# Kernel optimization log

Hardware: AMD Instinct MI355X
Metric: run time of the kernel (lower is better)

The kernel has to match this reference:

```python
import jax, jax.numpy as jnp
import numpy as np


def _resize_hw(x, h, w):
    # PyTorch F.interpolate(mode='bilinear', align_corners=False) == half-pixel
    # bilinear without antialiasing.
    return jax.image.resize(x, x.shape[:-2] + (h, w), method='bilinear', antialias=False)


def _make_char_mask(attn, fore_mask, alpha):
    # attn: [b,26,w_attn] float; fore_mask: [b,1,H,W] int32
    W = fore_mask.shape[-1]
    attn_i = _resize_hw(attn[:, None], 26, W)[:, 0]          # [b,26,W]
    attn_b = (attn_i > alpha).astype(jnp.int32)              # threshold
    single = attn_b[:, :, None, :] * fore_mask               # [b,26,H,W]
    return jnp.concatenate([1 - fore_mask, single], axis=1)  # [b,27,H,W]


def _loss(char_feature, mask, length):
    # char_feature: [b,27,H,W] logits; mask: [b,27,H,W] int; length: [b]
    c = char_feature.shape[1]
    target = jnp.argmax(mask, axis=1)                         # [b,H,W] (first-max, same as torch)
    logp = jax.nn.log_softmax(char_feature, axis=1)
    ce = -jnp.mean(jnp.take_along_axis(logp, target[:, None], axis=1))
    prob = jnp.exp(logp)
    m = mask.astype(prob.dtype)
    smooth = 1.0
    inter = jnp.sum(prob * m, axis=(2, 3))                    # [b,27]
    s1 = jnp.sum(prob, axis=(2, 3))
    s2 = jnp.sum(m, axis=(2, 3))
    score = (2.0 * inter + smooth) / (s1 + s2 + smooth)       # [b,27]
    lens = length - 1                                          # chars per sample
    ch = jnp.arange(c)
    valid = (ch[None, :] >= 1) & (ch[None, :] <= lens[:, None])  # channels 1..len
    per_sample = jnp.sum((1.0 - score) * valid, axis=1) / lens.astype(prob.dtype)
    dice = jnp.mean(per_sample)
    return ce + dice


def setup_inputs() -> dict:
    key = jax.random.key(0)
    k1, k2, k3, k4, k5 = jax.random.split(key, 5)
    b = 512
    return {
        'char_feature_mid': jax.random.normal(k1, (b, 27, 32, 128), dtype=jnp.float32),
        'char_feature_low': jax.random.normal(k2, (b, 27, 16, 64), dtype=jnp.float32),
        'seq1_attention_map': jax.random.uniform(k3, (b, 26, 32), dtype=jnp.float32),
        'fore_mask': jax.random.uniform(k4, (b, 1, 32, 128), dtype=jnp.float32),
        'length': jax.random.randint(k5, (b,), 2, 27),
        'alpha': jnp.float32(0.3),
    }


def reference(char_feature_mid, char_feature_low, seq1_attention_map, fore_mask, length, alpha):
    h_mid, w_mid = char_feature_mid.shape[-2:]
    h_low, w_low = char_feature_low.shape[-2:]
    # clear_noise: zero attention rows at index >= length-1
    keep = jnp.arange(seq1_attention_map.shape[1])[None, :] < (length - 1)[:, None]
    attn = seq1_attention_map * keep[..., None].astype(seq1_attention_map.dtype)
    # low-resolution branch
    fm_low = (_resize_hw(fore_mask, h_low, w_low) >= 0.4).astype(jnp.int32)
    mask_low = _make_char_mask(attn, fm_low, alpha)
    loss_low = _loss(char_feature_low, mask_low, length)
    # middle-resolution branch
    fm_mid = (_resize_hw(fore_mask, h_mid, w_mid) >= 0.4).astype(jnp.int32)
    mask_mid = _make_char_mask(attn, fm_mid, alpha)
    loss_middle = _loss(char_feature_mid, mask_mid, length)
    return ((loss_low, loss_middle), mask_low)
```

## Files before the change

### kernel.cpp

```cpp
#include <hip/hip_runtime.h>
#include <stdint.h>


static __device__ __forceinline__ float wave_reduce_add(float v) {
  v += __shfl_xor(v, 1, 64);
  v += __shfl_xor(v, 2, 64);
  v += __shfl_xor(v, 4, 64);
  v += __shfl_xor(v, 8, 64);
  v += __shfl_xor(v, 16, 64);
  v += __shfl_xor(v, 32, 64);
  return v;
}

static __device__ __forceinline__ uint32_t attn_bits(const float* sattn, float src,
                                                     int lens, float alpha) {
  const int k0 = (int)floorf(src);
  uint32_t bits = 0u;
  if (k0 < 0 || k0 >= 31) {
    const int kk = (k0 < 0) ? 0 : 31;
    for (int c = 0; c < 26; ++c) {
      float v = (c < lens) ? sattn[c * 32 + kk] : 0.0f;
      if (v > alpha) bits |= (1u << c);
    }
  } else {
    const float frac = src - (float)k0;
    const float w1 = frac, w0 = 1.0f - frac;
    for (int c = 0; c < 26; ++c) {
      float v = __fadd_rn(__fmul_rn(w0, sattn[c * 32 + k0]),
                          __fmul_rn(w1, sattn[c * 32 + k0 + 1]));
      v = (c < lens) ? v : 0.0f;
      if (v > alpha) bits |= (1u << c);
    }
  }
  return bits;
}

__global__ __launch_bounds__(192) void prep_kernel(
    const float* __restrict__ attn,
    const int* __restrict__ length,
    const float* __restrict__ alpha_p,
    uint32_t* __restrict__ bits_mid,
    uint32_t* __restrict__ bits_low,
    float* __restrict__ acc_mid,
    float* __restrict__ acc_low,
    float* __restrict__ ce) {
  __shared__ float sattn[26 * 32];
  const int b = blockIdx.x;
  const int t = threadIdx.x;
  for (int i = t; i < 832; i += 192) sattn[i] = attn[b * 832 + i];
  if (t < 81) { acc_mid[b * 81 + t] = 0.0f; acc_low[b * 81 + t] = 0.0f; }
  if (b == 0 && t >= 96 && t < 98) ce[t - 96] = 0.0f;
  __syncthreads();
  const float alpha = alpha_p[0];
  const int lens = length[b] - 1;
  if (t < 128) {
    const float src = 0.25f * (float)t - 0.375f;
    bits_mid[b * 128 + t] = attn_bits(sattn, src, lens, alpha);
  } else {
    const int x = t - 128;
    const float src = 0.5f * (float)x - 0.25f;
    bits_low[b * 64 + x] = attn_bits(sattn, src, lens, alpha);
  }
}

__global__ __launch_bounds__(256) void main_kernel(
    const float* __restrict__ cf_mid,
    const float* __restrict__ cf_low,
    const float* __restrict__ fore,
    float* __restrict__ out,
    const uint32_t* __restrict__ bits_mid,
    const uint32_t* __restrict__ bits_low,
    float* __restrict__ acc_mid,
    float* __restrict__ acc_low,
    float* __restrict__ ce) {
  const int t = threadIdx.x;
  const int bid = blockIdx.x;
  const bool low = (bid >= 4096);
  int b, p0, W, HW;
  const float* cf;
  const uint32_t* bitsp;
  float* acc;
  if (low) {
    const int idx = bid - 4096;
    b = idx >> 1; p0 = (idx & 1) << 9; W = 64; HW = 1024;
    cf = cf_low; bitsp = bits_low + (size_t)b * 64; acc = acc_low;
  } else {
    b = bid >> 3; p0 = (bid & 7) << 9; W = 128; HW = 4096;
    cf = cf_mid; bitsp = bits_mid + (size_t)b * 128; acc = acc_mid;
  }
  const float* cfb = cf + (size_t)b * 27 * HW;
  const float* fb = fore + (size_t)b * 4096;
  float* mout = out + 2 + (size_t)b * 27 * 1024;

  float inter[27], s1[27], s2[27];
#pragma unroll
  for (int c = 0; c < 27; ++c) { inter[c] = 0.0f; s1[c] = 0.0f; s2[c] = 0.0f; }
  float cesum = 0.0f;

  for (int k = 0; k < 2; ++k) {
    const int p = p0 + t + (k << 8);
    const int x = p & (W - 1);

    int fmw;
    if (low) {
      const int y = p >> 6;
      const float2* fr = (const float2*)(fb + (size_t)(2 * y) * 128 + 2 * x);
      const float2 f0 = fr[0];
      const float2 f1 = fr[64];
      const float t0 = __fadd_rn(0.5f * f0.x, 0.5f * f1.x);
      const float t1 = __fadd_rn(0.5f * f0.y, 0.5f * f1.y);
      const float fmv = __fadd_rn(0.5f * t0, 0.5f * t1);
      fmw = (fmv >= 0.4f) ? 1 : 0;
    } else {
      fmw = (fb[p] >= 0.4f) ? 1 : 0;
    }

    const uint32_t bits = bitsp[x];
    const int target = fmw ? (int)__ffs(bits) : 0;

    float l[27];
    float m = -1e30f, lt = 0.0f;
#pragma unroll
    for (int c = 0; c < 27; ++c) {
      const float v = cfb[(size_t)c * HW + p];
      l[c] = v;
      m = fmaxf(m, v);
      lt = (c == target) ? v : lt;
    }
    float s = 0.0f;
#pragma unroll
    for (int c = 0; c < 27; ++c) {
      const float e = __expf(l[c] - m);
      l[c] = e;
      s += e;
    }
    const float inv = 1.0f / s;
    cesum += (m + __logf(s) - lt);

#pragma unroll
    for (int c = 0; c < 27; ++c) {
      const float prob = l[c] * inv;
      s1[c] += prob;
      float mf;
      if (c == 0) mf = (float)(1 - fmw);
      else mf = (float)(((bits >> (c - 1)) & 1u) & (uint32_t)fmw);
      inter[c] += prob * mf;
      s2[c] += mf;
      if (low) mout[(size_t)c * 1024 + p] = mf;
    }
  }

  __shared__ float red[4][82];
  const int wave = t >> 6, lane = t & 63;
#pragma unroll
  for (int c = 0; c < 27; ++c) {
    inter[c] = wave_reduce_add(inter[c]);
    s1[c] = wave_reduce_add(s1[c]);
    s2[c] = wave_reduce_add(s2[c]);
  }
  cesum = wave_reduce_add(cesum);
  if (lane == 0) {
#pragma unroll
    for (int c = 0; c < 27; ++c) {
      red[wave][c] = inter[c];
      red[wave][27 + c] = s1[c];
      red[wave][54 + c] = s2[c];
    }
    red[wave][81] = cesum;
  }
  __syncthreads();
  if (t < 82) {
    const float v = red[0][t] + red[1][t] + red[2][t] + red[3][t];
    if (t == 81) atomicAdd(&ce[low ? 0 : 1], v);
    else atomicAdd(&acc[(size_t)b * 81 + t], v);
  }
}

__global__ __launch_bounds__(256) void final_kernel(
    const float* __restrict__ acc_mid,
    const float* __restrict__ acc_low,
    const float* __restrict__ ce,
    const int* __restrict__ length,
    float* __restrict__ out) {
  const int B = blockIdx.x;
  const float* acc = (B == 0) ? acc_low : acc_mid;
  const float hw = (B == 0) ? 1024.0f : 4096.0f;
  const int t = threadIdx.x;
  float dsum = 0.0f;
  for (int b = t; b < 512; b += 256) {
    const int lens = length[b] - 1;
    const float* a = acc + (size_t)b * 81;
    float d = 0.0f;
    for (int c = 1; c < 27; ++c) {
      const float I = a[c], S1 = a[27 + c], S2 = a[54 + c];
      const float score = (2.0f * I + 1.0f) / (S1 + S2 + 1.0f);
      if (c <= lens) d += (1.0f - score);
    }
    dsum += d / (float)lens;
  }
  __shared__ float red[4];
  const int wave = t >> 6, lane = t & 63;
  dsum = wave_reduce_add(dsum);
  if (lane == 0) red[wave] = dsum;
  __syncthreads();
  if (t == 0) {
    const float dice = red[0] + red[1] + red[2] + red[3];
    out[B] = dice * (1.0f / 512.0f) + ce[B] * (1.0f / (512.0f * hw));
  }
}

extern "C" void kernel_launch(void* const* d_in, const int* in_sizes, int n_in,
                              void* d_out, int out_size, void* d_ws, size_t ws_size,
                              hipStream_t stream) {
  const float* cf_mid = (const float*)d_in[0];
  const float* cf_low = (const float*)d_in[1];
  const float* attn   = (const float*)d_in[2];
  const float* fore   = (const float*)d_in[3];
  const int*   length = (const int*)d_in[4];
  const float* alpha  = (const float*)d_in[5];
  float* out = (float*)d_out;

  uint32_t* bits_mid = (uint32_t*)d_ws;
  uint32_t* bits_low = bits_mid + 512 * 128;
  float* acc_mid = (float*)(bits_low + 512 * 64);
  float* acc_low = acc_mid + 512 * 81;
  float* ce = acc_low + 512 * 81;

  hipLaunchKernelGGL(prep_kernel, dim3(512), dim3(192), 0, stream,
                     attn, length, alpha, bits_mid, bits_low, acc_mid, acc_low, ce);
  hipLaunchKernelGGL(main_kernel, dim3(5120), dim3(256), 0, stream,
                     cf_mid, cf_low, fore, out, bits_mid, bits_low,
                     acc_mid, acc_low, ce);
  hipLaunchKernelGGL(final_kernel, dim3(2), dim3(256), 0, stream,
                     acc_mid, acc_low, ce, length, out);
}
```

Measured before the change: 411.0 us.

## Precompute mask sums in prep, stage logits via LDS, drop max-subtraction in softmax

The s2 mask sums move into the prep kernel, which computes per-column foreground counts and combines them with the attention bitmasks, so the main kernel no longer accumulates s2. The main kernel now stages 256-pixel tiles of all 27 channels into shared memory with float4 loads. Each block covers 1024 pixels, and the grid is regrouped so that four mid blocks and one low block share a batch index. Softmax drops the max subtraction and uses a hardware reciprocal, which cuts ALU work but can overflow on large logits. The extra syncthreads per tile and the larger LDS footprint may limit occupancy.

```diff
diff --git a/kernel.cpp b/kernel.cpp
--- a/kernel.cpp
+++ b/kernel.cpp
@@ -35,8 +35,21 @@
   return bits;
 }
 
-__global__ __launch_bounds__(192) void prep_kernel(
+static __device__ __forceinline__ int fm_low_at(const float* fb, int p) {
+  const int y = p >> 6;
+  const int x = p & 63;
+  const float2* fr = (const float2*)(fb + (size_t)(2 * y) * 128 + 2 * x);
+  const float2 f0 = fr[0];
+  const float2 f1 = fr[64];
+  const float t0 = __fadd_rn(0.5f * f0.x, 0.5f * f1.x);
+  const float t1 = __fadd_rn(0.5f * f0.y, 0.5f * f1.y);
+  const float fmv = __fadd_rn(0.5f * t0, 0.5f * t1);
+  return (fmv >= 0.4f) ? 1 : 0;
+}
+
+__global__ __launch_bounds__(256) void prep_kernel(
     const float* __restrict__ attn,
+    const float* __restrict__ fore,
     const int* __restrict__ length,
     const float* __restrict__ alpha_p,
     uint32_t* __restrict__ bits_mid,
@@ -44,26 +57,62 @@
     float* __restrict__ acc_mid,
     float* __restrict__ acc_low,
     float* __restrict__ ce) {
-  __shared__ float sattn[26 * 32];
+  __shared__ float sattn[832];
+  __shared__ int colfm_m[128];
+  __shared__ int colfm_l[64];
+  __shared__ uint32_t sbm[128];
+  __shared__ uint32_t sbl[64];
   const int b = blockIdx.x;
   const int t = threadIdx.x;
-  for (int i = t; i < 832; i += 192) sattn[i] = attn[b * 832 + i];
-  if (t < 81) { acc_mid[b * 81 + t] = 0.0f; acc_low[b * 81 + t] = 0.0f; }
-  if (b == 0 && t >= 96 && t < 98) ce[t - 96] = 0.0f;
-  __syncthreads();
+  const float* fb = fore + (size_t)b * 4096;
+
+  for (int i = t; i < 832; i += 256) sattn[i] = attn[b * 832 + i];
+  if (t < 128) colfm_m[t] = 0;
+  if (t < 64) colfm_l[t] = 0;
+  __syncthreads();
+
+  int pm = 0;
+  for (int k = 0; k < 16; ++k) pm += (fb[t + 256 * k] >= 0.4f) ? 1 : 0;
+  atomicAdd(&colfm_m[t & 127], pm);
+  int pl = 0;
+  for (int k = 0; k < 4; ++k) pl += fm_low_at(fb, t + 256 * k);
+  atomicAdd(&colfm_l[t & 63], pl);
+
   const float alpha = alpha_p[0];
   const int lens = length[b] - 1;
   if (t < 128) {
-    const float src = 0.25f * (float)t - 0.375f;
-    bits_mid[b * 128 + t] = attn_bits(sattn, src, lens, alpha);
-  } else {
+    const uint32_t bm = attn_bits(sattn, 0.25f * (float)t - 0.375f, lens, alpha);
+    bits_mid[b * 128 + t] = bm;
+    sbm[t] = bm;
+  } else if (t < 192) {
     const int x = t - 128;
-    const float src = 0.5f * (float)x - 0.25f;
-    bits_low[b * 64 + x] = attn_bits(sattn, src, lens, alpha);
-  }
-}
-
-__global__ __launch_bounds__(256) void main_kernel(
+    const uint32_t bl = attn_bits(sattn, 0.5f * (float)x - 0.25f, lens, alpha);
+    bits_low[b * 64 + x] = bl;
+    sbl[x] = bl;
+  }
+  __syncthreads();
+
+  if (t < 54) { acc_mid[(size_t)b * 81 + t] = 0.0f; acc_low[(size_t)b * 81 + t] = 0.0f; }
+  if (t >= 64 && t < 91) {
+    const int c = t - 64;
+    int s2m = 0, s2l = 0;
+    if (c == 0) {
+      int tm = 0, tl = 0;
+      for (int x = 0; x < 128; ++x) tm += colfm_m[x];
+      for (int x = 0; x < 64; ++x) tl += colfm_l[x];
+      s2m = 4096 - tm;
+      s2l = 1024 - tl;
+    } else {
+      for (int x = 0; x < 128; ++x) s2m += colfm_m[x] * (int)((sbm[x] >> (c - 1)) & 1u);
+      for (int x = 0; x < 64; ++x) s2l += colfm_l[x] * (int)((sbl[x] >> (c - 1)) & 1u);
+    }
+    acc_mid[(size_t)b * 81 + 54 + c] = (float)s2m;
+    acc_low[(size_t)b * 81 + 54 + c] = (float)s2l;
+  }
+  if (b == 0 && t == 63) { ce[0] = 0.0f; ce[1] = 0.0f; }
+}
+
+__global__ __launch_bounds__(256, 4) void main_kernel(
     const float* __restrict__ cf_mid,
     const float* __restrict__ cf_low,
     const float* __restrict__ fore,
@@ -73,105 +122,98 @@
     float* __restrict__ acc_mid,
     float* __restrict__ acc_low,
     float* __restrict__ ce) {
+  __shared__ float s_tile[27 * 256];
+  __shared__ uint32_t s_bits[128];
+  __shared__ float red[4][55];
+
   const int t = threadIdx.x;
-  const int bid = blockIdx.x;
-  const bool low = (bid >= 4096);
-  int b, p0, W, HW;
+  const int g = blockIdx.x / 5;
+  const int r = blockIdx.x % 5;
+  const bool low = (r == 4);
+
+  int b, p0, HW;
   const float* cf;
-  const uint32_t* bitsp;
   float* acc;
   if (low) {
-    const int idx = bid - 4096;
-    b = idx >> 1; p0 = (idx & 1) << 9; W = 64; HW = 1024;
-    cf = cf_low; bitsp = bits_low + (size_t)b * 64; acc = acc_low;
+    b = g; p0 = 0; HW = 1024;
+    cf = cf_low; acc = acc_low;
   } else {
-    b = bid >> 3; p0 = (bid & 7) << 9; W = 128; HW = 4096;
-    cf = cf_mid; bitsp = bits_mid + (size_t)b * 128; acc = acc_mid;
+    const int idx = g * 4 + r;
+    b = idx >> 2; p0 = (idx & 3) << 10; HW = 4096;
+    cf = cf_mid; acc = acc_mid;
   }
   const float* cfb = cf + (size_t)b * 27 * HW;
   const float* fb = fore + (size_t)b * 4096;
   float* mout = out + 2 + (size_t)b * 27 * 1024;
 
-  float inter[27], s1[27], s2[27];
-#pragma unroll
-  for (int c = 0; c < 27; ++c) { inter[c] = 0.0f; s1[c] = 0.0f; s2[c] = 0.0f; }
+  if (t < (low ? 64 : 128))
+    s_bits[t] = (low ? bits_low + (size_t)b * 64 : bits_mid + (size_t)b * 128)[t];
+
+  float inter[27], s1[27];
+#pragma unroll
+  for (int c = 0; c < 27; ++c) { inter[c] = 0.0f; s1[c] = 0.0f; }
   float cesum = 0.0f;
 
-  for (int k = 0; k < 2; ++k) {
-    const int p = p0 + t + (k << 8);
-    const int x = p & (W - 1);
-
-    int fmw;
-    if (low) {
-      const int y = p >> 6;
-      const float2* fr = (const float2*)(fb + (size_t)(2 * y) * 128 + 2 * x);
-      const float2 f0 = fr[0];
-      const float2 f1 = fr[64];
-      const float t0 = __fadd_rn(0.5f * f0.x, 0.5f * f1.x);
-      const float t1 = __fadd_rn(0.5f * f0.y, 0.5f * f1.y);
-      const float fmv = __fadd_rn(0.5f * t0, 0.5f * t1);
-      fmw = (fmv >= 0.4f) ? 1 : 0;
-    } else {
-      fmw = (fb[p] >= 0.4f) ? 1 : 0;
-    }
-
-    const uint32_t bits = bitsp[x];
+  const int wv = t >> 6, ln = t & 63;
+  const int xmask = low ? 63 : 127;
+
+  for (int j = 0; j < 4; ++j) {
+    const int tp0 = p0 + (j << 8);
+    for (int c = wv; c < 27; c += 4) {
+      const float4 v = *(const float4*)(cfb + (size_t)c * HW + tp0 + 4 * ln);
+      *(float4*)&s_tile[c * 256 + 4 * ln] = v;
+    }
+    __syncthreads();
+
+    const int p = tp0 + t;
+    const uint32_t bits = s_bits[t & xmask];
+    const int fmw = low ? fm_low_at(fb, p) : ((fb[p] >= 0.4f) ? 1 : 0);
     const int target = fmw ? (int)__ffs(bits) : 0;
 
-    float l[27];
-    float m = -1e30f, lt = 0.0f;
+    float e[27];
+    float z = 0.0f, lt = 0.0f;
 #pragma unroll
     for (int c = 0; c < 27; ++c) {
-      const float v = cfb[(size_t)c * HW + p];
-      l[c] = v;
-      m = fmaxf(m, v);
+      const float v = s_tile[c * 256 + t];
       lt = (c == target) ? v : lt;
-    }
-    float s = 0.0f;
+      const float ee = __expf(v);
+      e[c] = ee;
+      z += ee;
+    }
+    const float inv = __builtin_amdgcn_rcpf(z);
+    cesum += (__logf(z) - lt);
+
 #pragma unroll
     for (int c = 0; c < 27; ++c) {
-      const float e = __expf(l[c] - m);
-      l[c] = e;
-      s += e;
-    }
-    const float inv = 1.0f / s;
-    cesum += (m + __logf(s) - lt);
-
-#pragma unroll
-    for (int c = 0; c < 27; ++c) {
-      const float prob = l[c] * inv;
+      const float prob = e[c] * inv;
       s1[c] += prob;
       float mf;
       if (c == 0) mf = (float)(1 - fmw);
       else mf = (float)(((bits >> (c - 1)) & 1u) & (uint32_t)fmw);
-      inter[c] += prob * mf;
-      s2[c] += mf;
+      inter[c] = __fmaf_rn(prob, mf, inter[c]);
       if (low) mout[(size_t)c * 1024 + p] = mf;
     }
-  }
-
-  __shared__ float red[4][82];
-  const int wave = t >> 6, lane = t & 63;
+    __syncthreads();
+  }
+
 #pragma unroll
   for (int c = 0; c < 27; ++c) {
     inter[c] = wave_reduce_add(inter[c]);
     s1[c] = wave_reduce_add(s1[c]);
-    s2[c] = wave_reduce_add(s2[c]);
   }
   cesum = wave_reduce_add(cesum);
-  if (lane == 0) {
+  if (ln == 0) {
 #pragma unroll
     for (int c = 0; c < 27; ++c) {
-      red[wave][c] = inter[c];
-      red[wave][27 + c] = s1[c];
-      red[wave][54 + c] = s2[c];
-    }
-    red[wave][81] = cesum;
-  }
-  __syncthreads();
-  if (t < 82) {
+      red[wv][c] = inter[c];
+      red[wv][27 + c] = s1[c];
+    }
+    red[wv][54] = cesum;
+  }
+  __syncthreads();
+  if (t < 55) {
     const float v = red[0][t] + red[1][t] + red[2][t] + red[3][t];
-    if (t == 81) atomicAdd(&ce[low ? 0 : 1], v);
+    if (t == 54) atomicAdd(&ce[low ? 0 : 1], v);
     else atomicAdd(&acc[(size_t)b * 81 + t], v);
   }
 }
@@ -226,9 +268,10 @@
   float* acc_low = acc_mid + 512 * 81;
   float* ce = acc_low + 512 * 81;
 
-  hipLaunchKernelGGL(prep_kernel, dim3(512), dim3(192), 0, stream,
-                     attn, length, alpha, bits_mid, bits_low, acc_mid, acc_low, ce);
-  hipLaunchKernelGGL(main_kernel, dim3(5120), dim3(256), 0, stream,
+  hipLaunchKernelGGL(prep_kernel, dim3(512), dim3(256), 0, stream,
+                     attn, fore, length, alpha, bits_mid, bits_low,
+                     acc_mid, acc_low, ce);
+  hipLaunchKernelGGL(main_kernel, dim3(2560), dim3(256), 0, stream,
                      cf_mid, cf_low, fore, out, bits_mid, bits_low,
                      acc_mid, acc_low, ce);
   hipLaunchKernelGGL(final_kernel, dim3(2), dim3(256), 0, stream,
```

Measured after the change: 480.0 us. 16.8% more time.
